# Kernel optimization log

Measured on AMD Instinct MI355X. Metric: run time of the kernel, lower is better.

## Reference

```python
import jax, jax.numpy as jnp
import numpy as np

DIM = 768
HEADS = 12


def setup_inputs() -> dict:
    key = jax.random.key(0)
    ks = jax.random.split(key, 7)
    bs, nmm, nv, na = 32, 256, 196, 60
    s = DIM ** -0.5
    return {
        "xmm": jax.random.normal(ks[0], (bs, nmm, DIM), jnp.float32),
        "xv": jax.random.normal(ks[1], (bs, nv, DIM), jnp.float32),
        "xa": jax.random.normal(ks[2], (bs, na, DIM), jnp.float32),
        "Wq": jax.random.normal(ks[3], (DIM, DIM), jnp.float32) * s,
        "Wkv": jax.random.normal(ks[4], (DIM, 2 * DIM), jnp.float32) * s,
        "Wproj": jax.random.normal(ks[5], (DIM, DIM), jnp.float32) * s,
        "bproj": jnp.zeros((DIM,), jnp.float32),
    }


def reference(xmm, xv, xa, Wq, Wkv, Wproj, bproj):
    bs, nmm, dim = xmm.shape
    hd = dim // HEADS
    scale = hd ** -0.5
    x_src = jnp.concatenate([xv, xa], axis=1)            # [bs, nv+na, dim]
    q = (xmm @ Wq).reshape(bs, nmm, HEADS, hd).transpose(0, 2, 1, 3)   # [b,h,q,d]
    kv = (x_src @ Wkv).reshape(bs, -1, 2, HEADS, hd).transpose(2, 0, 3, 1, 4)
    k, v = kv[0], kv[1]                                  # [b,h,k,d]
    attn = jax.nn.softmax(jnp.einsum('bhqd,bhkd->bhqk', q, k) * scale, axis=-1)
    out = jnp.einsum('bhqk,bhkd->bhqd', attn, v)
    out = out.transpose(0, 2, 1, 3).reshape(bs, nmm, dim)
    out = out @ Wproj + bproj
    return out, attn
```

## Files before the change

### kernel.cpp

```cpp
#include <hip/hip_runtime.h>


typedef __attribute__((ext_vector_type(8))) _Float16 f16x8;
typedef __attribute__((ext_vector_type(4))) _Float16 f16x4;
typedef __attribute__((ext_vector_type(4))) float    f32x4;

#define AS1 __attribute__((address_space(1)))
#define AS3 __attribute__((address_space(3)))

__device__ __forceinline__ void gload_lds16(const void* g, void* l) {
    void* gnc = const_cast<void*>(g);
    __builtin_amdgcn_global_load_lds((AS1 void*)gnc, (AS3 void*)l, 16, 0, 0);
}

__global__ __launch_bounds__(256) void prep_all(const float* __restrict__ xmm,
                                                const float* __restrict__ xv,
                                                const float* __restrict__ xa,
                                                const float* __restrict__ Wq,
                                                const float* __restrict__ Wkv,
                                                const float* __restrict__ Wproj,
                                                _Float16* __restrict__ xmm16,
                                                _Float16* __restrict__ xsrc16,
                                                _Float16* __restrict__ WqT,
                                                _Float16* __restrict__ WkvT,
                                                _Float16* __restrict__ WprojT) {
    __shared__ _Float16 wlds[64][72];
    int bid = blockIdx.x;
    if (bid < 12288) {
        int id = bid * 256 + threadIdx.x;
        float4 v;
        _Float16* dst;
        int off;
        if (id < 1572864) {
            v = ((const float4*)xmm)[id];
            dst = xmm16; off = id;
        } else {
            int t = id - 1572864;
            int c4 = t % 192;
            int r  = (t / 192) & 255;
            int b  = t / 49152;
            if (r < 196) v = ((const float4*)xv)[((long)b * 196 + r) * 192 + c4];
            else         v = ((const float4*)xa)[((long)b * 60 + (r - 196)) * 192 + c4];
            dst = xsrc16; off = t;
        }
        f16x4 h = { (_Float16)v.x, (_Float16)v.y, (_Float16)v.z, (_Float16)v.w };
        ((f16x4*)dst)[off] = h;
        return;
    }
    int t = bid - 12288;
    const float* src; _Float16* dst; int W; float scale; int tk, tn;
    if (t < 144)      { src = Wq;    dst = WqT;    W = 768;  scale = 0.125f; tk = t % 12;  tn = t / 12; }
    else if (t < 432) { int u = t - 144; src = Wkv;   dst = WkvT;   W = 1536; scale = 1.0f; tk = u % 12; tn = u / 12; }
    else              { int u = t - 432; src = Wproj; dst = WprojT; W = 768;  scale = 1.0f; tk = u % 12; tn = u / 12; }
    const int tk0 = tk * 64, tn0 = tn * 64;
    const int rloc = threadIdx.x >> 4, c0 = (threadIdx.x & 15) * 4;
#pragma unroll
    for (int i = 0; i < 4; ++i) {
        int k = tk0 + rloc + 16 * i;
        float4 v = *(const float4*)(src + (long)k * W + tn0 + c0);
        wlds[c0 + 0][rloc + 16 * i] = (_Float16)(v.x * scale);
        wlds[c0 + 1][rloc + 16 * i] = (_Float16)(v.y * scale);
        wlds[c0 + 2][rloc + 16 * i] = (_Float16)(v.z * scale);
        wlds[c0 + 3][rloc + 16 * i] = (_Float16)(v.w * scale);
    }
    __syncthreads();
#pragma unroll
    for (int i = 0; i < 4; ++i) {
        int nloc = rloc + 16 * i;
        f16x4 h = *(const f16x4*)(&wlds[nloc][c0]);
        *(f16x4*)(dst + (long)(tn0 + nloc) * 768 + tk0 + c0) = h;
    }
}

template <int OUT_F32>
__device__ __forceinline__ void gemm_body(const _Float16* __restrict__ A,
                                          const _Float16* __restrict__ Bt,
                                          void* __restrict__ C,
                                          const float* __restrict__ bias,
                                          long bm, long bn, int N, int K) {
    __shared__ _Float16 As[128 * 64];
    __shared__ _Float16 Bs[128 * 64];

    const int tid  = threadIdx.x;
    const int wave = tid >> 6, lane = tid & 63;
    const int lrow = lane & 15, quad = lane >> 4;
    const int wm = (wave >> 1) * 64, wn = (wave & 1) * 64;

    f32x4 acc[4][4];
    const f32x4 fz = {0.f, 0.f, 0.f, 0.f};
#pragma unroll
    for (int mt = 0; mt < 4; ++mt)
#pragma unroll
        for (int nt = 0; nt < 4; ++nt) acc[mt][nt] = fz;

    for (int k0 = 0; k0 < K; k0 += 64) {
#pragma unroll
        for (int it = 0; it < 4; ++it) {
            int seg = tid + it * 256;
            int rr = seg >> 3, pp = seg & 7;
            int cc = ((pp ^ (rr & 7)) << 3);
            gload_lds16(A  + (bm + rr) * (long)K + k0 + cc, As + seg * 8);
            gload_lds16(Bt + (bn + rr) * (long)K + k0 + cc, Bs + seg * 8);
        }
        __syncthreads();
#pragma unroll
        for (int ks = 0; ks < 2; ++ks) {
            f16x8 af[4], bf[4];
#pragma unroll
            for (int mt = 0; mt < 4; ++mt) {
                int r = wm + mt * 16 + lrow;
                af[mt] = *(const f16x8*)(As + r * 64 + (((ks * 4 + quad) ^ (r & 7)) << 3));
            }
#pragma unroll
            for (int nt = 0; nt < 4; ++nt) {
                int r = wn + nt * 16 + lrow;
                bf[nt] = *(const f16x8*)(Bs + r * 64 + (((ks * 4 + quad) ^ (r & 7)) << 3));
            }
#pragma unroll
            for (int mt = 0; mt < 4; ++mt)
#pragma unroll
                for (int nt = 0; nt < 4; ++nt)
                    acc[mt][nt] = __builtin_amdgcn_mfma_f32_16x16x32_f16(
                        bf[nt], af[mt], acc[mt][nt], 0, 0, 0);
        }
        __syncthreads();
    }

#pragma unroll
    for (int mt = 0; mt < 4; ++mt) {
        long row = bm + wm + mt * 16 + lrow;
#pragma unroll
        for (int nt = 0; nt < 4; ++nt) {
            long col0 = bn + wn + nt * 16 + quad * 4;
            if (OUT_F32) {
                float4 b4 = *(const float4*)(bias + col0);
                float4 o = { acc[mt][nt][0] + b4.x, acc[mt][nt][1] + b4.y,
                             acc[mt][nt][2] + b4.z, acc[mt][nt][3] + b4.w };
                *(float4*)((float*)C + row * N + col0) = o;
            } else {
                f16x4 h = { (_Float16)acc[mt][nt][0], (_Float16)acc[mt][nt][1],
                            (_Float16)acc[mt][nt][2], (_Float16)acc[mt][nt][3] };
                *(f16x4*)((_Float16*)C + row * N + col0) = h;
            }
        }
    }
}

__global__ __launch_bounds__(256, 2)
void gemm_qkv(const _Float16* __restrict__ xmm16, const _Float16* __restrict__ xsrc16,
              const _Float16* __restrict__ WqT, const _Float16* __restrict__ WkvT,
              _Float16* __restrict__ Q16, _Float16* __restrict__ KV16) {
    const int f = blockIdx.x;
    const int w = ((f & 7) * 144) + (f >> 3);
    const int bx = w % 18;
    const long bm = (long)(w / 18) * 128;
    if (bx < 6) gemm_body<0>(xmm16,  WqT,  (void*)Q16,  nullptr, bm, (long)bx * 128,       768,  768);
    else        gemm_body<0>(xsrc16, WkvT, (void*)KV16, nullptr, bm, (long)(bx - 6) * 128, 1536, 768);
}

__global__ __launch_bounds__(256, 2)
void gemm_proj(const _Float16* __restrict__ O16, const _Float16* __restrict__ WprojT,
               float* __restrict__ out, const float* __restrict__ bias) {
    const int f = blockIdx.x;
    const int w = ((f & 7) * 48) + (f >> 3);
    const int bx = w % 6;
    const long bm = (long)(w / 6) * 128;
    gemm_body<1>(O16, WprojT, (void*)out, bias, bm, (long)bx * 128, 768, 768);
}

__global__ __launch_bounds__(256, 2)
void attn_kernel(const _Float16* __restrict__ Qg, const _Float16* __restrict__ KVg,
                 float* __restrict__ attn_out, _Float16* __restrict__ Og) {
    __shared__ _Float16 sh[32768];
    _Float16* Ks = sh;
    _Float16* Vt = sh + 16384;
    _Float16* Ps = sh;

    const int tid  = threadIdx.x;
    const int wave = tid >> 6, lane = tid & 63;
    const int lrow = lane & 15, quad = lane >> 4;
    const int f = blockIdx.x;
    const int w = ((f & 7) * 192) + (f >> 3);
    const int qb = w & 3;
    const int hb = w >> 2;
    const int h = hb % 12, b = hb / 12;
    const long qrow0 = (long)b * 256 + qb * 64;
    const long krow0 = (long)b * 256;

    f16x8 aq[2];
#pragma unroll
    for (int ks = 0; ks < 2; ++ks)
        aq[ks] = *(const f16x8*)(Qg + (qrow0 + wave * 16 + lrow) * 768 + h * 64 + ks * 32 + quad * 8);

#pragma unroll
    for (int it = 0; it < 8; ++it) {
        int seg = tid + it * 256;
        int rr = seg >> 3, pp = seg & 7;
        int cc = ((pp ^ (rr & 7)) << 3);
        gload_lds16(KVg + (krow0 + rr) * 1536 + h * 64 + cc, Ks + seg * 8);
    }
#pragma unroll
    for (int it = 0; it < 8; ++it) {
        int seg = tid + it * 256;
        int key = seg >> 3, d0 = (seg & 7) * 8;
        f16x8 v = *(const f16x8*)(KVg + (krow0 + key) * 1536 + 768 + h * 64 + d0);
#pragma unroll
        for (int i = 0; i < 8; ++i) {
            int d = d0 + i;
            Vt[d * 256 + ((((key >> 3) ^ (d & 7)) << 3) | (key & 7))] = v[i];
        }
    }
    __syncthreads();

    f32x4 sacc[16];
    const f32x4 fz = {0.f, 0.f, 0.f, 0.f};
#pragma unroll
    for (int nt = 0; nt < 16; ++nt) sacc[nt] = fz;
#pragma unroll
    for (int ks = 0; ks < 2; ++ks) {
#pragma unroll
        for (int nt = 0; nt < 16; ++nt) {
            int r = nt * 16 + lrow;
            f16x8 bk = *(const f16x8*)(Ks + r * 64 + (((ks * 4 + quad) ^ (r & 7)) << 3));
            sacc[nt] = __builtin_amdgcn_mfma_f32_16x16x32_f16(bk, aq[ks], sacc[nt], 0, 0, 0);
        }
    }

    float m = -1e30f;
#pragma unroll
    for (int nt = 0; nt < 16; ++nt)
#pragma unroll
        for (int j = 0; j < 4; ++j) m = fmaxf(m, sacc[nt][j]);
    m = fmaxf(m, __shfl_xor(m, 16));
    m = fmaxf(m, __shfl_xor(m, 32));
    float s = 0.f;
#pragma unroll
    for (int nt = 0; nt < 16; ++nt)
#pragma unroll
        for (int j = 0; j < 4; ++j) {
            float p = __expf(sacc[nt][j] - m);
            sacc[nt][j] = p; s += p;
        }
    s += __shfl_xor(s, 16);
    s += __shfl_xor(s, 32);
    const float li = 1.f / s;

    __syncthreads();

    const long abase = (((long)b * 12 + h) * 256 + qb * 64) * 256;
    const int q = wave * 16 + lrow;
#pragma unroll
    for (int nt = 0; nt < 16; ++nt) {
        float4 o = { sacc[nt][0] * li, sacc[nt][1] * li, sacc[nt][2] * li, sacc[nt][3] * li };
        *(float4*)(attn_out + abase + (long)q * 256 + nt * 16 + quad * 4) = o;
        f16x4 hp = { (_Float16)o.x, (_Float16)o.y, (_Float16)o.z, (_Float16)o.w };
        int blk = nt * 2 + (quad >> 1);
        *(f16x4*)(Ps + q * 256 + ((blk ^ (q & 7)) << 3) + ((quad & 1) << 2)) = hp;
    }
    asm volatile("s_waitcnt lgkmcnt(0)" ::: "memory");
    __builtin_amdgcn_sched_barrier(0);
    __builtin_amdgcn_s_barrier();

    f32x4 oacc[4];
#pragma unroll
    for (int nt = 0; nt < 4; ++nt) oacc[nt] = fz;
#pragma unroll
    for (int ks = 0; ks < 8; ++ks) {
        int pr = wave * 16 + lrow;
        f16x8 ap = *(const f16x8*)(Ps + pr * 256 + (((ks * 4 + quad) ^ (pr & 7)) << 3));
#pragma unroll
        for (int nt = 0; nt < 4; ++nt) {
            int d = nt * 16 + lrow;
            f16x8 bv = *(const f16x8*)(Vt + d * 256 + (((ks * 4 + quad) ^ (d & 7)) << 3));
            oacc[nt] = __builtin_amdgcn_mfma_f32_16x16x32_f16(bv, ap, oacc[nt], 0, 0, 0);
        }
    }
#pragma unroll
    for (int nt = 0; nt < 4; ++nt) {
        f16x4 ho = { (_Float16)oacc[nt][0], (_Float16)oacc[nt][1],
                     (_Float16)oacc[nt][2], (_Float16)oacc[nt][3] };
        *(f16x4*)(Og + (qrow0 + wave * 16 + lrow) * 768 + h * 64 + nt * 16 + quad * 4) = ho;
    }
}

extern "C" void kernel_launch(void* const* d_in, const int* in_sizes, int n_in,
                              void* d_out, int out_size, void* d_ws, size_t ws_size,
                              hipStream_t stream) {
    const float* xmm   = (const float*)d_in[0];
    const float* xv    = (const float*)d_in[1];
    const float* xa    = (const float*)d_in[2];
    const float* Wq    = (const float*)d_in[3];
    const float* Wkv   = (const float*)d_in[4];
    const float* Wproj = (const float*)d_in[5];
    const float* bproj = (const float*)d_in[6];

    float* out  = (float*)d_out;
    float* attn = out + 6291456;

    char* ws = (char*)d_ws;
    _Float16* xmm16  = (_Float16*)(ws);
    _Float16* xsrc16 = (_Float16*)(ws + 12582912);
    _Float16* WqT    = (_Float16*)(ws + 25165824);
    _Float16* WkvT   = (_Float16*)(ws + 26345472);
    _Float16* WprojT = (_Float16*)(ws + 28704768);
    _Float16* Q16    = (_Float16*)(ws + 29884416);
    _Float16* KV16   = (_Float16*)(ws + 42467328);
    _Float16* O16    = xmm16;

    prep_all<<<12864, 256, 0, stream>>>(xmm, xv, xa, Wq, Wkv, Wproj,
                                        xmm16, xsrc16, WqT, WkvT, WprojT);

    gemm_qkv<<<1152, 256, 0, stream>>>(xmm16, xsrc16, WqT, WkvT, Q16, KV16);

    attn_kernel<<<1536, 256, 0, stream>>>(Q16, KV16, attn, O16);

    gemm_proj<<<384, 256, 0, stream>>>(O16, WprojT, out, bproj);
}
```

Before: 271.3 us.

## Stream K/V through a half-size LDS buffer to fit three attention blocks per CU

Shrinks the attention kernel's shared memory from 64KB to 48KB. K and V now pass through a single 16KB buffer in two 128-key halves, with V halves held in registers and transposed into LDS between phases. Launch bounds rise to three blocks per CU to raise occupancy. In exchange it adds several block barriers, more register pressure from the V staging registers, and less overlap of global loads with compute.

```diff
diff --git a/kernel.cpp b/kernel.cpp
--- a/kernel.cpp
+++ b/kernel.cpp
@@ -168,13 +168,12 @@
     gemm_body<1>(O16, WprojT, (void*)out, bias, bm, (long)bx * 128, 768, 768);
 }
 
-__global__ __launch_bounds__(256, 2)
+__global__ __launch_bounds__(256, 3)
 void attn_kernel(const _Float16* __restrict__ Qg, const _Float16* __restrict__ KVg,
                  float* __restrict__ attn_out, _Float16* __restrict__ Og) {
-    __shared__ _Float16 sh[32768];
-    _Float16* Ks = sh;
-    _Float16* Vt = sh + 16384;
-    _Float16* Ps = sh;
+    __shared__ _Float16 sh[24576];
+    _Float16* KVbuf = sh;
+    _Float16* Ps    = sh + 8192;
 
     const int tid  = threadIdx.x;
     const int wave = tid >> 6, lane = tid & 63;
@@ -193,24 +192,14 @@
         aq[ks] = *(const f16x8*)(Qg + (qrow0 + wave * 16 + lrow) * 768 + h * 64 + ks * 32 + quad * 8);
 
 #pragma unroll
-    for (int it = 0; it < 8; ++it) {
+    for (int it = 0; it < 4; ++it) {
         int seg = tid + it * 256;
         int rr = seg >> 3, pp = seg & 7;
         int cc = ((pp ^ (rr & 7)) << 3);
-        gload_lds16(KVg + (krow0 + rr) * 1536 + h * 64 + cc, Ks + seg * 8);
-    }
-#pragma unroll
-    for (int it = 0; it < 8; ++it) {
-        int seg = tid + it * 256;
-        int key = seg >> 3, d0 = (seg & 7) * 8;
-        f16x8 v = *(const f16x8*)(KVg + (krow0 + key) * 1536 + 768 + h * 64 + d0);
-#pragma unroll
-        for (int i = 0; i < 8; ++i) {
-            int d = d0 + i;
-            Vt[d * 256 + ((((key >> 3) ^ (d & 7)) << 3) | (key & 7))] = v[i];
-        }
-    }
-    __syncthreads();
+        gload_lds16(KVg + (krow0 + rr) * 1536 + h * 64 + cc, KVbuf + seg * 8);
+    }
+    asm volatile("s_waitcnt vmcnt(0)" ::: "memory");
+    __builtin_amdgcn_s_barrier();
 
     f32x4 sacc[16];
     const f32x4 fz = {0.f, 0.f, 0.f, 0.f};
@@ -219,12 +208,43 @@
 #pragma unroll
     for (int ks = 0; ks < 2; ++ks) {
 #pragma unroll
-        for (int nt = 0; nt < 16; ++nt) {
+        for (int nt = 0; nt < 8; ++nt) {
             int r = nt * 16 + lrow;
-            f16x8 bk = *(const f16x8*)(Ks + r * 64 + (((ks * 4 + quad) ^ (r & 7)) << 3));
+            f16x8 bk = *(const f16x8*)(KVbuf + r * 64 + (((ks * 4 + quad) ^ (r & 7)) << 3));
             sacc[nt] = __builtin_amdgcn_mfma_f32_16x16x32_f16(bk, aq[ks], sacc[nt], 0, 0, 0);
         }
     }
+    __builtin_amdgcn_s_barrier();
+
+#pragma unroll
+    for (int it = 0; it < 4; ++it) {
+        int seg = tid + it * 256;
+        int rr = seg >> 3, pp = seg & 7;
+        int cc = ((pp ^ (rr & 7)) << 3);
+        gload_lds16(KVg + (krow0 + 128 + rr) * 1536 + h * 64 + cc, KVbuf + seg * 8);
+    }
+    f16x8 v0r[4], v1r[4];
+#pragma unroll
+    for (int it = 0; it < 4; ++it) {
+        int seg = tid + it * 256;
+        int key_l = seg >> 3, d0 = (seg & 7) * 8;
+        v0r[it] = *(const f16x8*)(KVg + (krow0 + key_l) * 1536 + 768 + h * 64 + d0);
+        v1r[it] = *(const f16x8*)(KVg + (krow0 + 128 + key_l) * 1536 + 768 + h * 64 + d0);
+    }
+    asm volatile("s_waitcnt vmcnt(0)" ::: "memory");
+    __builtin_amdgcn_s_barrier();
+
+#pragma unroll
+    for (int ks = 0; ks < 2; ++ks) {
+#pragma unroll
+        for (int nt = 8; nt < 16; ++nt) {
+            int r = nt * 16 + lrow;
+            int rl = r - 128;
+            f16x8 bk = *(const f16x8*)(KVbuf + rl * 64 + (((ks * 4 + quad) ^ (rl & 7)) << 3));
+            sacc[nt] = __builtin_amdgcn_mfma_f32_16x16x32_f16(bk, aq[ks], sacc[nt], 0, 0, 0);
+        }
+    }
+    __builtin_amdgcn_s_barrier();
 
     float m = -1e30f;
 #pragma unroll
@@ -245,7 +265,16 @@
     s += __shfl_xor(s, 32);
     const float li = 1.f / s;
 
-    __syncthreads();
+#pragma unroll
+    for (int it = 0; it < 4; ++it) {
+        int seg = tid + it * 256;
+        int key_l = seg >> 3, d0 = (seg & 7) * 8;
+#pragma unroll
+        for (int i = 0; i < 8; ++i) {
+            int d = d0 + i;
+            KVbuf[d * 128 + (((key_l >> 3) ^ (d & 7)) << 3) + (key_l & 7)] = v0r[it][i];
+        }
+    }
 
     const long abase = (((long)b * 12 + h) * 256 + qb * 64) * 256;
     const int q = wave * 16 + lrow;
@@ -264,14 +293,40 @@
     f32x4 oacc[4];
 #pragma unroll
     for (int nt = 0; nt < 4; ++nt) oacc[nt] = fz;
-#pragma unroll
-    for (int ks = 0; ks < 8; ++ks) {
-        int pr = wave * 16 + lrow;
+    const int pr = wave * 16 + lrow;
+#pragma unroll
+    for (int ks = 0; ks < 4; ++ks) {
         f16x8 ap = *(const f16x8*)(Ps + pr * 256 + (((ks * 4 + quad) ^ (pr & 7)) << 3));
 #pragma unroll
         for (int nt = 0; nt < 4; ++nt) {
             int d = nt * 16 + lrow;
-            f16x8 bv = *(const f16x8*)(Vt + d * 256 + (((ks * 4 + quad) ^ (d & 7)) << 3));
+            f16x8 bv = *(const f16x8*)(KVbuf + d * 128 + ((((ks & 3) * 4 + quad) ^ (d & 7)) << 3));
+            oacc[nt] = __builtin_amdgcn_mfma_f32_16x16x32_f16(bv, ap, oacc[nt], 0, 0, 0);
+        }
+    }
+    __builtin_amdgcn_s_barrier();
+
+#pragma unroll
+    for (int it = 0; it < 4; ++it) {
+        int seg = tid + it * 256;
+        int key_l = seg >> 3, d0 = (seg & 7) * 8;
+#pragma unroll
+        for (int i = 0; i < 8; ++i) {
+            int d = d0 + i;
+            KVbuf[d * 128 + (((key_l >> 3) ^ (d & 7)) << 3) + (key_l & 7)] = v1r[it][i];
+        }
+    }
+    asm volatile("s_waitcnt lgkmcnt(0)" ::: "memory");
+    __builtin_amdgcn_sched_barrier(0);
+    __builtin_amdgcn_s_barrier();
+
+#pragma unroll
+    for (int ks = 4; ks < 8; ++ks) {
+        f16x8 ap = *(const f16x8*)(Ps + pr * 256 + (((ks * 4 + quad) ^ (pr & 7)) << 3));
+#pragma unroll
+        for (int nt = 0; nt < 4; ++nt) {
+            int d = nt * 16 + lrow;
+            f16x8 bv = *(const f16x8*)(KVbuf + d * 128 + ((((ks & 3) * 4 + quad) ^ (d & 7)) << 3));
             oacc[nt] = __builtin_amdgcn_mfma_f32_16x16x32_f16(bv, ap, oacc[nt], 0, 0, 0);
         }
     }
```

After: 264.8 us. 1.02x faster.
